# Kernel tuning notes

Measured on AMD Instinct MI355X. Metric: run time of the kernel, lower is better.

The kernel has to match this reference:

```python
import jax, jax.numpy as jnp
import numpy as np

B, M, K, KNN = 2, 256, 64, 16
CXYZ, CFEAT = 3, 61
CIN = CXYZ + CFEAT  # 64
MLPS = [64, 128]
SUMM = sum(MLPS)    # 192
CALIB = 64
EXP = [256, 512]
OUT = 256
EPS = 1e-5


def bn(x, g, b):
    # BatchNorm eval mode with running_mean=0, running_var=1 (channel axis 1)
    shape = (1, -1) + (1,) * (x.ndim - 2)
    return x * (g / jnp.sqrt(1.0 + EPS)).reshape(shape) + b.reshape(shape)


def knn(x, k):
    xx = jnp.sum(x * x, axis=1)                      # (B, N)
    inner = jnp.einsum('bcn,bcm->bnm', x, x)         # (B, N, N)
    pd = 2.0 * inner - xx[:, :, None] - xx[:, None, :]
    return jax.lax.top_k(pd, k)[1]                   # (B, N, k)


def graph_feature(x, idx):
    # x: (B, C, N), idx: (B, N, k) -> (B, 2C, N, k)
    xt = jnp.transpose(x, (0, 2, 1))                 # (B, N, C)
    nb = jax.vmap(lambda a, i: a[i])(xt, idx)        # (B, N, k, C)
    ctr = xt[:, :, None, :]
    feat = jnp.concatenate([nb - ctr, jnp.broadcast_to(ctr, nb.shape)], axis=-1)
    return jnp.transpose(feat, (0, 3, 1, 2))


def forward(xyz, feats, e1_w, e1_g, e1_b, e2_w, e2_g, e2_b,
            cal1_w, cal1_g, cal1_b, cal2_w, cal2_bias,
            exp1_w, exp1_g, exp1_b, exp2_w, exp2_g, exp2_b,
            red_w, red_g, red_b, sc1_w, sc1_b, sc2_w, sc2_b,
            sc_n1_g, sc_n1_b, sc_n2_g, sc_n2_b):
    x3 = xyz.reshape(B * M, K, CXYZ).transpose(0, 2, 1)      # (BM, 3, K)
    f = feats.reshape(B * M, K, CFEAT).transpose(0, 2, 1)    # (BM, 61, K)
    idx = knn(x3, KNN)                                        # USE_FEATS_DIS=False: knn once on xyz
    x = jnp.concatenate([x3, f], axis=1)                      # (BM, 64, K)
    outs = []
    for W, g, b in ((e1_w, e1_g, e1_b), (e2_w, e2_g, e2_b)):
        gf = graph_feature(x, idx)                            # (BM, 2C, K, knn)
        y = jax.nn.relu(bn(jnp.einsum('oc,bcnk->bonk', W, gf), g, b))
        x = y.max(axis=-1)                                    # (BM, mlp_i, K)
        outs.append(x)
    x = jnp.concatenate(outs, axis=1)                         # (BM, 192, K)
    c = jax.nn.relu(bn(jnp.einsum('oc,bcn->bon', cal1_w, x), cal1_g, cal1_b))
    c = jnp.einsum('oc,bcn->bon', cal2_w, c) + cal2_bias[None, :, None]
    x = jax.nn.sigmoid(c) * x
    x = jax.nn.relu(bn(jnp.einsum('oc,bcn->bon', exp1_w, x), exp1_g, exp1_b))
    x = jax.nn.relu(bn(jnp.einsum('oc,bcn->bon', exp2_w, x), exp2_g, exp2_b))
    x = x.max(axis=-1).reshape(B, M, EXP[1]).transpose(0, 2, 1)  # (B, 512, M)
    x = jax.nn.relu(bn(jnp.einsum('oc,bcm->bom', red_w, x), red_g, red_b))
    x = bn(x + x, sc_n1_g, sc_n1_b)
    h = jax.nn.relu(jnp.einsum('oc,bcm->bom', sc1_w, x) + sc1_b[None, :, None])
    h = jnp.einsum('oc,bcm->bom', sc2_w, h) + sc2_b[None, :, None]
    x = bn(x + h, sc_n2_g, sc_n2_b)
    return x                                                  # (B, 256, M)


def setup_inputs() -> dict:
    key = jax.random.key(0)
    ks = jax.random.split(key, 16)
    w = lambda k, s: jax.random.normal(k, s, jnp.float32) * 0.05
    ones = lambda n: jnp.ones((n,), jnp.float32)
    zeros = lambda n: jnp.zeros((n,), jnp.float32)
    return {
        'xyz': jax.random.normal(ks[0], (B, M, K, CXYZ), jnp.float32),
        'feats': jax.random.normal(ks[1], (B, M, K, CFEAT), jnp.float32),
        'e1_w': w(ks[2], (MLPS[0], 2 * CIN)), 'e1_g': ones(MLPS[0]), 'e1_b': zeros(MLPS[0]),
        'e2_w': w(ks[3], (MLPS[1], 2 * MLPS[0])), 'e2_g': ones(MLPS[1]), 'e2_b': zeros(MLPS[1]),
        'cal1_w': w(ks[4], (CALIB, SUMM)), 'cal1_g': ones(CALIB), 'cal1_b': zeros(CALIB),
        'cal2_w': w(ks[5], (SUMM, CALIB)), 'cal2_bias': zeros(SUMM),
        'exp1_w': w(ks[6], (EXP[0], SUMM)), 'exp1_g': ones(EXP[0]), 'exp1_b': zeros(EXP[0]),
        'exp2_w': w(ks[7], (EXP[1], EXP[0])), 'exp2_g': ones(EXP[1]), 'exp2_b': zeros(EXP[1]),
        'red_w': w(ks[8], (OUT, EXP[1])), 'red_g': ones(OUT), 'red_b': zeros(OUT),
        'sc1_w': w(ks[9], (OUT, OUT)), 'sc1_b': zeros(OUT),
        'sc2_w': w(ks[10], (OUT, OUT)), 'sc2_b': zeros(OUT),
        'sc_n1_g': ones(OUT), 'sc_n1_b': zeros(OUT),
        'sc_n2_g': ones(OUT), 'sc_n2_b': zeros(OUT),
    }


def reference(xyz, feats, e1_w, e1_g, e1_b, e2_w, e2_g, e2_b,
              cal1_w, cal1_g, cal1_b, cal2_w, cal2_bias,
              exp1_w, exp1_g, exp1_b, exp2_w, exp2_g, exp2_b,
              red_w, red_g, red_b, sc1_w, sc1_b, sc2_w, sc2_b,
              sc_n1_g, sc_n1_b, sc_n2_g, sc_n2_b):
    return forward(xyz, feats, e1_w, e1_g, e1_b, e2_w, e2_g, e2_b,
                   cal1_w, cal1_g, cal1_b, cal2_w, cal2_bias,
                   exp1_w, exp1_g, exp1_b, exp2_w, exp2_g, exp2_b,
                   red_w, red_g, red_b, sc1_w, sc1_b, sc2_w, sc2_b,
                   sc_n1_g, sc_n1_b, sc_n2_g, sc_n2_b)
```

## Files before the change

kernel.cpp:

```cpp
#include <hip/hip_runtime.h>
#include <hip/hip_bf16.h>
#include <math.h>
#include <stddef.h>

#define DEV __device__ __forceinline__
__device__ const float BNS = 0.99999500003749968f;

typedef __bf16 bf16x8 __attribute__((ext_vector_type(8)));
typedef float  f32x4  __attribute__((ext_vector_type(4)));

DEV unsigned short f2bs(float v){
  union{ __hip_bfloat16 b; unsigned short u; } c; c.b=__float2bfloat16(v); return c.u;
}
DEV float bs2f(unsigned short u){
  union{ unsigned short u; __hip_bfloat16 b; } c; c.u=u; return __bfloat162float(c.b);
}


__global__ __launch_bounds__(256) void k_prep(const float* __restrict__ e1_w,
    const float* __restrict__ e2_w, const float* __restrict__ cal1_w,
    const float* __restrict__ cal2_w, const float* __restrict__ exp1_w,
    const float* __restrict__ exp2_w, unsigned short* __restrict__ Whi,
    unsigned short* __restrict__ Wlo,
    const float* __restrict__ red_w, const float* __restrict__ sc1_w,
    const float* __restrict__ sc2_w, float* __restrict__ Wt_red,
    float* __restrict__ Wt_s1, float* __restrict__ Wt_s2){
  __shared__ float s[32][33];
  int bid = blockIdx.x;
  if(bid < 896){
    const float* src; unsigned short *hi,*lo; int mode, O=0, i0;
    if(bid<32)      { src=e1_w;  hi=Whi;       lo=Wlo;       mode=1; O= 64; i0=bid*256; }
    else if(bid<96) { src=e2_w;  hi=Whi+8192;  lo=Wlo+8192;  mode=1; O=128; i0=(bid-32)*256; }
    else if(bid<144){ src=cal1_w;hi=Whi+24576; lo=Wlo+24576; mode=0;        i0=(bid-96)*256; }
    else if(bid<192){ src=cal2_w;hi=Whi+36864; lo=Wlo+36864; mode=0;        i0=(bid-144)*256; }
    else if(bid<384){ src=exp1_w;hi=Whi+49152; lo=Wlo+49152; mode=0;        i0=(bid-192)*256; }
    else            { src=exp2_w;hi=Whi+98304; lo=Wlo+98304; mode=0;        i0=(bid-384)*256; }
    int i = i0 + threadIdx.x;
    float v;
    if(mode==0) v = src[i];
    else {
      int row=i>>6, c=i&63;
      v = (row<O) ? src[row*128+c] : (src[(row-O)*128+64+c]-src[(row-O)*128+c]);
    }
    unsigned short h=f2bs(v); hi[i]=h; lo[i]=f2bs(v-bs2f(h));
  } else {
    int lb = bid-896;
    const float* in; float* out; int O,K;
    if(lb<128){ in=red_w; out=Wt_red; O=256; K=512; }
    else if(lb<192){ in=sc1_w; out=Wt_s1; O=256; K=256; lb-=128; }
    else { in=sc2_w; out=Wt_s2; O=256; K=256; lb-=192; }
    int nt=O>>5;
    int to=lb%nt, tk=lb/nt;
    int c=threadIdx.x&31, r8=threadIdx.x>>5;
    #pragma unroll
    for(int p=0;p<4;p++){
      int r=r8+p*8;
      s[r][c]=in[(size_t)(to*32+r)*K + tk*32 + c];
    }
    __syncthreads();
    #pragma unroll
    for(int p=0;p<4;p++){
      int r=r8+p*8;
      out[(size_t)(tk*32+r)*O + to*32 + c]=s[c][r];
    }
  }
}

__global__ __launch_bounds__(256) void k_knne12(const float* __restrict__ xyz,
    const float* __restrict__ feats,
    const unsigned short* __restrict__ W1h, const unsigned short* __restrict__ W1l,
    const unsigned short* __restrict__ W2h, const unsigned short* __restrict__ W2l,
    int* __restrict__ idxo, const float* __restrict__ g1, const float* __restrict__ b1,
    const float* __restrict__ g2, const float* __restrict__ b2,
    unsigned short* __restrict__ cat){
  __shared__ float bufA[64*65];
  __shared__ float bufB[64*65];
  __shared__ __align__(16) unsigned short sb[64*136];
  __shared__ int   ips[64*16];
  __shared__ float sx0[64], sx1[64], sx2[64], sxx[64];
  int bm = blockIdx.x;
  int tid = threadIdx.x, n = tid&63, s = tid>>6;
  int wid = tid>>6, lane = tid&63;
  int l15 = lane&15, q = lane>>4;
  if(s==0){
    const float* xp = xyz + (size_t)(bm*64+n)*3;
    float px=xp[0], py=xp[1], pz=xp[2];
    sx0[n]=px; sx1[n]=py; sx2[n]=pz; sxx[n]=px*px+py*py+pz*pz;
  }
  __syncthreads();
  {
    int p = lane>>2, seg = lane&3;
    int n1 = wid*16 + p;
    float px=sx0[n1], py=sx1[n1], pz=sx2[n1], xxn=sxx[n1];
    float pdr[16];
    #pragma unroll
    for(int t=0;t<16;t++){
      int m = seg*16+t;
      pdr[t] = 2.f*(px*sx0[m]+py*sx1[m]+pz*sx2[m]) - xxn - sxx[m];
    }
    for(int j=0;j<16;j++){
      float bv=-3.4e38f; int bi=seg*16;
      #pragma unroll
      for(int t=0;t<16;t++){ if(pdr[t]>bv){bv=pdr[t]; bi=seg*16+t;} }
      float ov=__shfl_xor(bv,1); int oi=__shfl_xor(bi,1);
      if(ov>bv || (ov==bv && oi<bi)){bv=ov;bi=oi;}
      ov=__shfl_xor(bv,2); oi=__shfl_xor(bi,2);
      if(ov>bv || (ov==bv && oi<bi)){bv=ov;bi=oi;}
      if(seg==0) ips[n1*16+j]=bi;
      if((bi>>4)==seg) pdr[bi&15]=-3.4e38f;
    }
  }
  {
    unsigned short* r = sb + n*136;
    if(s==0){
      float px=sx0[n], py=sx1[n], pz=sx2[n];
      unsigned short h;
      h=f2bs(px); r[0]=h; r[64]=f2bs(px-bs2f(h));
      h=f2bs(py); r[1]=h; r[65]=f2bs(py-bs2f(h));
      h=f2bs(pz); r[2]=h; r[66]=f2bs(pz-bs2f(h));
    }
    const float* fp = feats + (size_t)(bm*64+n)*61;
    #pragma unroll
    for(int t=0;t<16;t++){
      int cc = s*16+t;
      if(cc<61){
        float v=fp[cc]; unsigned short h=f2bs(v);
        r[3+cc]=h; r[64+3+cc]=f2bs(v-bs2f(h));
      }
    }
  }
  __syncthreads();
  #pragma unroll
  for(int t=0;t<4;t++) idxo[bm*1024 + tid*4 + t] = ips[tid*4 + t];
  {
    int rbase = ((wid<2)?0:64) + (wid&1)*32;
    f32x4 acc[2][4];
    #pragma unroll
    for(int a=0;a<2;a++)
      #pragma unroll
      for(int d=0;d<4;d++) acc[a][d]=(f32x4){0.f,0.f,0.f,0.f};
    #pragma unroll
    for(int kc=0;kc<2;kc++){
      int k0=kc*32;
      size_t a0=(size_t)(rbase+l15)*64 + k0 + q*8;
      size_t a1=(size_t)(rbase+16+l15)*64 + k0 + q*8;
      bf16x8 a0h=*(const bf16x8*)(W1h+a0), a0l=*(const bf16x8*)(W1l+a0);
      bf16x8 a1h=*(const bf16x8*)(W1h+a1), a1l=*(const bf16x8*)(W1l+a1);
      #pragma unroll
      for(int nt=0;nt<4;nt++){
        int row = nt*16 + l15;
        bf16x8 bh = *(const bf16x8*)&sb[row*136 + k0 + q*8];
        bf16x8 bl = *(const bf16x8*)&sb[row*136 + 64 + k0 + q*8];
        acc[0][nt]=__builtin_amdgcn_mfma_f32_16x16x32_bf16(a0h,bh,acc[0][nt],0,0,0);
        acc[0][nt]=__builtin_amdgcn_mfma_f32_16x16x32_bf16(a0h,bl,acc[0][nt],0,0,0);
        acc[0][nt]=__builtin_amdgcn_mfma_f32_16x16x32_bf16(a0l,bh,acc[0][nt],0,0,0);
        acc[1][nt]=__builtin_amdgcn_mfma_f32_16x16x32_bf16(a1h,bh,acc[1][nt],0,0,0);
        acc[1][nt]=__builtin_amdgcn_mfma_f32_16x16x32_bf16(a1h,bl,acc[1][nt],0,0,0);
        acc[1][nt]=__builtin_amdgcn_mfma_f32_16x16x32_bf16(a1l,bh,acc[1][nt],0,0,0);
      }
    }
    __syncthreads();
    float* dst = (wid<2)? bufA : bufB;
    int ro = (wid&1)*32;
    #pragma unroll
    for(int mt=0;mt<2;mt++)
      #pragma unroll
      for(int nt=0;nt<4;nt++)
        #pragma unroll
        for(int rr=0;rr<4;rr++)
          dst[(ro+mt*16+q*4+rr)*65 + nt*16+l15] = acc[mt][nt][rr];
  }
  __syncthreads();
  {
    int o = lane;
    float sc = g1[o]*BNS, bi = b1[o];
    #pragma unroll 4
    for(int j=0;j<16;j++){
      int nn = wid*16 + j;
      const int* ip = &ips[nn*16];
      float mz = -3.4e38f;
      #pragma unroll
      for(int k=0;k<16;k++) mz = fmaxf(mz, bufA[o*65 + ip[k]]);
      float v = fmaxf(sc*(mz + bufB[o*65 + nn]) + bi, 0.f);
      unsigned short hv = f2bs(v), lv = f2bs(v - bs2f(hv));
      size_t cb = ((size_t)bm*64+nn)*384 + o;
      cat[cb] = hv; cat[cb+192] = lv;
      sb[nn*136 + o] = hv; sb[nn*136 + 64 + o] = lv;
    }
  }
  for(int ch=0; ch<2; ch++){
    __syncthreads();
    int rbase = ((wid<2)?0:128) + ch*64 + (wid&1)*32;
    f32x4 acc[2][4];
    #pragma unroll
    for(int a=0;a<2;a++)
      #pragma unroll
      for(int d=0;d<4;d++) acc[a][d]=(f32x4){0.f,0.f,0.f,0.f};
    #pragma unroll
    for(int kc=0;kc<2;kc++){
      int k0=kc*32;
      size_t a0=(size_t)(rbase+l15)*64 + k0 + q*8;
      size_t a1=(size_t)(rbase+16+l15)*64 + k0 + q*8;
      bf16x8 a0h=*(const bf16x8*)(W2h+a0), a0l=*(const bf16x8*)(W2l+a0);
      bf16x8 a1h=*(const bf16x8*)(W2h+a1), a1l=*(const bf16x8*)(W2l+a1);
      #pragma unroll
      for(int nt=0;nt<4;nt++){
        int row = nt*16 + l15;
        bf16x8 bh = *(const bf16x8*)&sb[row*136 + k0 + q*8];
        bf16x8 bl = *(const bf16x8*)&sb[row*136 + 64 + k0 + q*8];
        acc[0][nt]=__builtin_amdgcn_mfma_f32_16x16x32_bf16(a0h,bh,acc[0][nt],0,0,0);
        acc[0][nt]=__builtin_amdgcn_mfma_f32_16x16x32_bf16(a0h,bl,acc[0][nt],0,0,0);
        acc[0][nt]=__builtin_amdgcn_mfma_f32_16x16x32_bf16(a0l,bh,acc[0][nt],0,0,0);
        acc[1][nt]=__builtin_amdgcn_mfma_f32_16x16x32_bf16(a1h,bh,acc[1][nt],0,0,0);
        acc[1][nt]=__builtin_amdgcn_mfma_f32_16x16x32_bf16(a1h,bl,acc[1][nt],0,0,0);
        acc[1][nt]=__builtin_amdgcn_mfma_f32_16x16x32_bf16(a1l,bh,acc[1][nt],0,0,0);
      }
    }
    __syncthreads();
    float* dst = (wid<2)? bufA : bufB;
    int ro = (wid&1)*32;
    #pragma unroll
    for(int mt=0;mt<2;mt++)
      #pragma unroll
      for(int nt=0;nt<4;nt++)
        #pragma unroll
        for(int rr=0;rr<4;rr++)
          dst[(ro+mt*16+q*4+rr)*65 + nt*16+l15] = acc[mt][nt][rr];
    __syncthreads();
    int o = ch*64 + lane;
    float sc = g2[o]*BNS, bi = b2[o];
    #pragma unroll 4
    for(int j=0;j<16;j++){
      int nn = wid*16 + j;
      const int* ip = &ips[nn*16];
      float mz = -3.4e38f;
      #pragma unroll
      for(int k=0;k<16;k++) mz = fmaxf(mz, bufA[lane*65 + ip[k]]);
      float v = fmaxf(sc*(mz + bufB[lane*65 + nn]) + bi, 0.f);
      unsigned short hv = f2bs(v);
      size_t cb = ((size_t)bm*64+nn)*384 + 64 + o;
      cat[cb] = hv; cat[cb+192] = f2bs(v - bs2f(hv));
    }
  }
}

__global__ __launch_bounds__(256) void k_cal(
    const unsigned short* __restrict__ Whi, const unsigned short* __restrict__ Wlo,
    unsigned short* __restrict__ cats,
    const float* __restrict__ c1g, const float* __restrict__ c1b,
    const float* __restrict__ c2bias){
  const unsigned short* c1w_h = Whi+24576; const unsigned short* c1w_l = Wlo+24576;
  const unsigned short* c2w_h = Whi+36864; const unsigned short* c2w_l = Wlo+36864;
  __shared__ __align__(16) unsigned short sW[64*64];
  __shared__ __align__(16) unsigned short sX[128*64];
  __shared__ __align__(16) unsigned short c1L[128*136];
  int rt = blockIdx.x;
  int tid = threadIdx.x, wid = tid>>6, lane = tid&63;
  int l15 = lane&15, q = lane>>4;
  f32x4 acc1[8];
  #pragma unroll
  for(int d=0;d<8;d++) acc1[d]=(f32x4){0.f,0.f,0.f,0.f};
  size_t xbase = (size_t)rt*128*384;
  for(int kc=0;kc<6;kc++){
    int k0=kc*32;
    __syncthreads();
    #pragma unroll
    for(int i=0;i<2;i++){
      int U = tid + i*256;
      int r = U>>3, up = U&7, u = up ^ (r&7);
      const unsigned short* src = (u<4)
        ? (c1w_h + (size_t)r*192 + k0 + u*8)
        : (c1w_l + (size_t)r*192 + k0 + (u-4)*8);
      *(uint4*)&sW[U*8] = *(const uint4*)src;
    }
    #pragma unroll
    for(int i=0;i<4;i++){
      int U = tid + i*256;
      int r = U>>3, up = U&7, u = up ^ (r&7);
      const unsigned short* src = cats + xbase + (size_t)r*384
        + (u<4 ? (size_t)(k0 + u*8) : (size_t)(192 + k0 + (u-4)*8));
      *(uint4*)&sX[U*8] = *(const uint4*)src;
    }
    __syncthreads();
    int o = wid*16 + l15;
    bf16x8 wh = *(const bf16x8*)&sW[(o*8 + ((  q) ^ (o&7)))*8];
    bf16x8 wl = *(const bf16x8*)&sW[(o*8 + ((4+q) ^ (o&7)))*8];
    #pragma unroll
    for(int nf=0;nf<8;nf++){
      int r = nf*16 + l15;
      bf16x8 xh = *(const bf16x8*)&sX[(r*8 + ((  q) ^ (r&7)))*8];
      bf16x8 xl = *(const bf16x8*)&sX[(r*8 + ((4+q) ^ (r&7)))*8];
      acc1[nf]=__builtin_amdgcn_mfma_f32_16x16x32_bf16(wh,xh,acc1[nf],0,0,0);
      acc1[nf]=__builtin_amdgcn_mfma_f32_16x16x32_bf16(wh,xl,acc1[nf],0,0,0);
      acc1[nf]=__builtin_amdgcn_mfma_f32_16x16x32_bf16(wl,xh,acc1[nf],0,0,0);
    }
  }
  {
    int ob0 = wid*16 + q*4;
    float s0[4], b0[4];
    #pragma unroll
    for(int r=0;r<4;r++){ s0[r]=c1g[ob0+r]*BNS; b0[r]=c1b[ob0+r]; }
    #pragma unroll
    for(int nf=0;nf<8;nf++){
      int n = nf*16 + l15;
      unsigned short hv[4], lv[4];
      #pragma unroll
      for(int r=0;r<4;r++){
        float v = fmaxf(acc1[nf][r]*s0[r]+b0[r], 0.f);
        hv[r]=f2bs(v); lv[r]=f2bs(v - bs2f(hv[r]));
      }
      *(ushort4*)&c1L[n*136 + ob0]      = make_ushort4(hv[0],hv[1],hv[2],hv[3]);
      *(ushort4*)&c1L[n*136 + 64 + ob0] = make_ushort4(lv[0],lv[1],lv[2],lv[3]);
    }
  }
  __syncthreads();
  f32x4 acc2[3][8];
  #pragma unroll
  for(int a=0;a<3;a++)
    #pragma unroll
    for(int d=0;d<8;d++) acc2[a][d]=(f32x4){0.f,0.f,0.f,0.f};
  #pragma unroll
  for(int kc=0;kc<2;kc++){
    int k0=kc*32;
    bf16x8 ah[3], al[3];
    #pragma unroll
    for(int mt=0;mt<3;mt++){
      int o = wid*48 + mt*16 + l15;
      ah[mt]=*(const bf16x8*)(c2w_h + (size_t)o*64 + k0 + q*8);
      al[mt]=*(const bf16x8*)(c2w_l + (size_t)o*64 + k0 + q*8);
    }
    #pragma unroll
    for(int nf=0;nf<8;nf++){
      int n = nf*16 + l15;
      bf16x8 bh = *(const bf16x8*)&c1L[n*136 + k0 + q*8];
      bf16x8 bl = *(const bf16x8*)&c1L[n*136 + 64 + k0 + q*8];
      #pragma unroll
      for(int mt=0;mt<3;mt++){
        acc2[mt][nf]=__builtin_amdgcn_mfma_f32_16x16x32_bf16(ah[mt],bh,acc2[mt][nf],0,0,0);
        acc2[mt][nf]=__builtin_amdgcn_mfma_f32_16x16x32_bf16(ah[mt],bl,acc2[mt][nf],0,0,0);
        acc2[mt][nf]=__builtin_amdgcn_mfma_f32_16x16x32_bf16(al[mt],bh,acc2[mt][nf],0,0,0);
      }
    }
  }
  #pragma unroll
  for(int mt=0;mt<3;mt++){
    int ob0 = wid*48 + mt*16 + q*4;
    float bi[4];
    #pragma unroll
    for(int r=0;r<4;r++) bi[r]=c2bias[ob0+r];
    #pragma unroll
    for(int nf=0;nf<8;nf++){
      size_t row = (size_t)rt*128 + nf*16 + l15;
      size_t rb = row*384;
      ushort4 hv = *(ushort4*)(cats + rb + ob0);
      ushort4 lv = *(ushort4*)(cats + rb + 192 + ob0);
      unsigned short h[4]={hv.x,hv.y,hv.z,hv.w}, l[4]={lv.x,lv.y,lv.z,lv.w};
      #pragma unroll
      for(int r=0;r<4;r++){
        float g = 1.f/(1.f+__expf(-(acc2[mt][nf][r]+bi[r])));
        float f = (bs2f(h[r])+bs2f(l[r]))*g;
        h[r]=f2bs(f); l[r]=f2bs(f-bs2f(h[r]));
      }
      *(ushort4*)(cats + rb + ob0)       = make_ushort4(h[0],h[1],h[2],h[3]);
      *(ushort4*)(cats + rb + 192 + ob0) = make_ushort4(l[0],l[1],l[2],l[3]);
    }
  }
}

template<int K, int BO, int EPI>
__global__ __launch_bounds__(256) void k_mm2(
    const unsigned short* __restrict__ Whi, const unsigned short* __restrict__ Wlo,
    const unsigned short* __restrict__ X, void* __restrict__ Og,
    const float* __restrict__ sg, const float* __restrict__ bg, int O){
  constexpr int WO = BO/4;
  constexpr int MT = WO/16;
  constexpr int WUNITS = BO*8;
  __shared__ __align__(16) unsigned short sW[BO*64];
  __shared__ __align__(16) unsigned short sX[128*64];
  int rt = blockIdx.x;
  int o0 = blockIdx.y*BO;
  int tid = threadIdx.x, wid = tid>>6, lane = tid&63;
  int l15 = lane&15, q = lane>>4;
  f32x4 acc[MT][8];
  #pragma unroll
  for(int a=0;a<MT;a++)
    #pragma unroll
    for(int d=0;d<8;d++) acc[a][d]=(f32x4){0.f,0.f,0.f,0.f};
  size_t xbase = (size_t)rt*128*2*K;
  for(int kc=0; kc<K/32; kc++){
    int k0 = kc*32;
    __syncthreads();
    #pragma unroll
    for(int i=0;i<WUNITS/256;i++){
      int U = tid + i*256;
      int r = U>>3, up = U&7, u = up ^ (r&7);
      const unsigned short* src = (u<4)
        ? (Whi + (size_t)(o0+r)*K + k0 + u*8)
        : (Wlo + (size_t)(o0+r)*K + k0 + (u-4)*8);
      *(uint4*)&sW[U*8] = *(const uint4*)src;
    }
    #pragma unroll
    for(int i=0;i<4;i++){
      int U = tid + i*256;
      int r = U>>3, up = U&7, u = up ^ (r&7);
      const unsigned short* src = X + xbase + (size_t)r*2*K
        + (u<4 ? (size_t)(k0 + u*8) : (size_t)(K + k0 + (u-4)*8));
      *(uint4*)&sX[U*8] = *(const uint4*)src;
    }
    __syncthreads();
    bf16x8 wf[MT][2];
    #pragma unroll
    for(int mt=0;mt<MT;mt++){
      int o = wid*WO + mt*16 + l15;
      wf[mt][0] = *(const bf16x8*)&sW[(o*8 + ((  q) ^ (o&7)))*8];
      wf[mt][1] = *(const bf16x8*)&sW[(o*8 + ((4+q) ^ (o&7)))*8];
    }
    #pragma unroll
    for(int nf=0;nf<8;nf++){
      int r = nf*16 + l15;
      bf16x8 xh = *(const bf16x8*)&sX[(r*8 + ((  q) ^ (r&7)))*8];
      bf16x8 xl = *(const bf16x8*)&sX[(r*8 + ((4+q) ^ (r&7)))*8];
      #pragma unroll
      for(int mt=0;mt<MT;mt++){
        acc[mt][nf]=__builtin_amdgcn_mfma_f32_16x16x32_bf16(wf[mt][0],xh,acc[mt][nf],0,0,0);
        acc[mt][nf]=__builtin_amdgcn_mfma_f32_16x16x32_bf16(wf[mt][0],xl,acc[mt][nf],0,0,0);
        acc[mt][nf]=__builtin_amdgcn_mfma_f32_16x16x32_bf16(wf[mt][1],xh,acc[mt][nf],0,0,0);
      }
    }
  }
  if(EPI==0){
    unsigned short* ob = (unsigned short*)Og;
    #pragma unroll
    for(int mt=0;mt<MT;mt++){
      int ob0 = o0 + wid*WO + mt*16 + q*4;
      float s0[4], b0[4];
      #pragma unroll
      for(int r=0;r<4;r++){ s0[r]=sg[ob0+r]*BNS; b0[r]=bg[ob0+r]; }
      #pragma unroll
      for(int nf=0;nf<8;nf++){
        size_t row = (size_t)rt*128 + nf*16 + l15;
        size_t rb = row*2*O;
        unsigned short hv[4], lv[4];
        #pragma unroll
        for(int r=0;r<4;r++){
          float v = fmaxf(acc[mt][nf][r]*s0[r]+b0[r], 0.f);
          hv[r]=f2bs(v); lv[r]=f2bs(v - bs2f(hv[r]));
        }
        *(ushort4*)(ob + rb + ob0)     = make_ushort4(hv[0],hv[1],hv[2],hv[3]);
        *(ushort4*)(ob + rb + O + ob0) = make_ushort4(lv[0],lv[1],lv[2],lv[3]);
      }
    }
  } else {
    float* pool = (float*)Og;
    #pragma unroll
    for(int mt=0;mt<MT;mt++){
      int ob0 = o0 + wid*WO + mt*16 + q*4;
      #pragma unroll
      for(int half=0;half<2;half++){
        int bm = 2*rt + half;
        int b = bm>>8, m = bm&255;
        #pragma unroll
        for(int r=0;r<4;r++){
          float s=sg[ob0+r]*BNS, bi=bg[ob0+r];
          float v = acc[mt][half*4+0][r]*s+bi;
          v = fmaxf(v, acc[mt][half*4+1][r]*s+bi);
          v = fmaxf(v, acc[mt][half*4+2][r]*s+bi);
          v = fmaxf(v, acc[mt][half*4+3][r]*s+bi);
          v = fmaxf(v, 0.f);
          v = fmaxf(v, __shfl_xor(v,1));
          v = fmaxf(v, __shfl_xor(v,2));
          v = fmaxf(v, __shfl_xor(v,4));
          v = fmaxf(v, __shfl_xor(v,8));
          if(l15==0) pool[((size_t)b*512 + ob0+r)*256 + m] = v;
        }
      }
    }
  }
}

template<int EPI>
__global__ __launch_bounds__(256) void k_head(const float* __restrict__ Wt,
    const float* __restrict__ Xg, float* __restrict__ Og,
    const float* __restrict__ p0, const float* __restrict__ p1,
    const float* __restrict__ p2, const float* __restrict__ p3,
    const float* __restrict__ res, int O, int K){
  __shared__ float As[32][64];
  __shared__ float Bs[32][32];
  int not_ = O>>6;
  int g = blockIdx.x / not_, ot = blockIdx.x % not_;
  int b = g>>3, mg = g&7;
  int o0 = ot*64;
  int tid=threadIdx.x, tx=tid&7, ty=tid>>3;
  float acc[2][4];
  #pragma unroll
  for(int a=0;a<2;a++)
    #pragma unroll
    for(int d=0;d<4;d++) acc[a][d]=0.f;
  const float* Xb = Xg + (size_t)b*K*256 + mg*32;
  for(int k0=0;k0<K;k0+=32){
    __syncthreads();
    #pragma unroll
    for(int p=0;p<2;p++){
      int r = p*16 + (tid>>4), c4 = (tid&15)*4;
      *(float4*)&As[r][c4] = *(const float4*)&Wt[(size_t)(k0+r)*O + o0 + c4];
    }
    {
      int r = tid>>3, c4 = (tid&7)*4;
      *(float4*)&Bs[r][c4] = *(const float4*)&Xb[(size_t)(k0+r)*256 + c4];
    }
    __syncthreads();
    #pragma unroll
    for(int k=0;k<32;k++){
      float av[2], bv[4];
      av[0]=As[k][ty*2]; av[1]=As[k][ty*2+1];
      #pragma unroll
      for(int d=0;d<4;d++) bv[d]=Bs[k][tx*4+d];
      #pragma unroll
      for(int a=0;a<2;a++)
        #pragma unroll
        for(int d=0;d<4;d++) acc[a][d]+=av[a]*bv[d];
    }
  }
  int m0 = mg*32 + tx*4;
  #pragma unroll
  for(int a=0;a<2;a++){
    int o=o0+ty*2+a;
    float* orow = Og + ((size_t)b*O + o)*256 + m0;
    float v[4];
    if(EPI==0){
      float s=p0[o]*BNS, bi=p1[o], s1=p2[o]*BNS, b1=p3[o];
      #pragma unroll
      for(int d=0;d<4;d++){ float r=fmaxf(acc[a][d]*s+bi,0.f); v[d]=2.f*r*s1+b1; }
    } else if(EPI==1){
      float bi=p0[o];
      #pragma unroll
      for(int d=0;d<4;d++) v[d]=fmaxf(acc[a][d]+bi,0.f);
    } else {
      float bi=p0[o], s2=p1[o]*BNS, b2=p2[o];
      const float* rr = res + ((size_t)b*O + o)*256 + m0;
      #pragma unroll
      for(int d=0;d<4;d++){ float u=rr[d]+acc[a][d]+bi; v[d]=u*s2+b2; }
    }
    *(float4*)orow = make_float4(v[0],v[1],v[2],v[3]);
  }
}

extern "C" void kernel_launch(void* const* d_in, const int* in_sizes, int n_in,
                              void* d_out, int out_size, void* d_ws, size_t ws_size,
                              hipStream_t stream){
  const float* xyz     =(const float*)d_in[0];
  const float* feats   =(const float*)d_in[1];
  const float* e1_w    =(const float*)d_in[2];
  const float* e1_g    =(const float*)d_in[3];
  const float* e1_b    =(const float*)d_in[4];
  const float* e2_w    =(const float*)d_in[5];
  const float* e2_g    =(const float*)d_in[6];
  const float* e2_b    =(const float*)d_in[7];
  const float* cal1_w  =(const float*)d_in[8];
  const float* cal1_g  =(const float*)d_in[9];
  const float* cal1_b  =(const float*)d_in[10];
  const float* cal2_w  =(const float*)d_in[11];
  const float* cal2_bias=(const float*)d_in[12];
  const float* exp1_w  =(const float*)d_in[13];
  const float* exp1_g  =(const float*)d_in[14];
  const float* exp1_b  =(const float*)d_in[15];
  const float* exp2_w  =(const float*)d_in[16];
  const float* exp2_g  =(const float*)d_in[17];
  const float* exp2_b  =(const float*)d_in[18];
  const float* red_w   =(const float*)d_in[19];
  const float* red_g   =(const float*)d_in[20];
  const float* red_b   =(const float*)d_in[21];
  const float* sc1_w   =(const float*)d_in[22];
  const float* sc1_b   =(const float*)d_in[23];
  const float* sc2_w   =(const float*)d_in[24];
  const float* sc2_b   =(const float*)d_in[25];
  const float* sc_n1_g =(const float*)d_in[26];
  const float* sc_n1_b =(const float*)d_in[27];
  const float* sc_n2_g =(const float*)d_in[28];
  const float* sc_n2_b =(const float*)d_in[29];

  char* wsb=(char*)d_ws;
  int*            idx =(int*)           (wsb);
  unsigned short* cats=(unsigned short*)(wsb + 10485760);
  unsigned short* p1s =(unsigned short*)(wsb + 35651584);
  float*          pool=(float*)         (wsb + 69206016);
  float*          x1  =(float*)         (wsb + 70254592);
  float*          hbuf=(float*)         (wsb + 70778880);
  unsigned short* Whi =(unsigned short*)(wsb + 75497472);
  unsigned short* Wlo =(unsigned short*)(wsb + 76021760);
  float*          Wt_red=(float*)       (wsb + 76546048);
  float*          Wt_s1 =(float*)       (wsb + 77070336);
  float*          Wt_s2 =(float*)       (wsb + 77332480);
  unsigned short* e1e_h=Whi;          unsigned short* e1e_l=Wlo;
  unsigned short* e2e_h=Whi+8192;     unsigned short* e2e_l=Wlo+8192;
  unsigned short* e1w_h=Whi+49152;    unsigned short* e1w_l=Wlo+49152;
  unsigned short* e2w_h=Whi+98304;    unsigned short* e2w_l=Wlo+98304;

  k_prep      <<<1152,256,0,stream>>>(e1_w,e2_w,cal1_w,cal2_w,exp1_w,exp2_w,Whi,Wlo,
                                      red_w,sc1_w,sc2_w,Wt_red,Wt_s1,Wt_s2);
  k_knne12    <<<512,256,0,stream>>>(xyz,feats,e1e_h,e1e_l,e2e_h,e2e_l,idx,
                                     e1_g,e1_b,e2_g,e2_b,cats);
  k_cal       <<<256,256,0,stream>>>(Whi,Wlo,cats,cal1_g,cal1_b,cal2_bias);
  k_mm2<192,128,0><<<dim3(256,2),256,0,stream>>>(e1w_h,e1w_l,cats,(void*)p1s,exp1_g,exp1_b,256);
  k_mm2<256,128,2><<<dim3(256,4),256,0,stream>>>(e2w_h,e2w_l,p1s,(void*)pool,exp2_g,exp2_b,512);
  k_head<0>   <<< 64,256,0,stream>>>(Wt_red,pool,x1,  red_g,red_b,sc_n1_g,sc_n1_b,nullptr,256,512);
  k_head<1>   <<< 64,256,0,stream>>>(Wt_s1, x1,  hbuf,sc1_b,nullptr,nullptr,nullptr,nullptr,256,256);
  k_head<2>   <<< 64,256,0,stream>>>(Wt_s2, hbuf,(float*)d_out,sc2_b,sc_n2_g,sc_n2_b,nullptr,x1,256,256);
}
```

Before: 267.8 us.

## Fuse three head GEMM kernels into one per-column-group kernel

Replaces the three k_head launches (reduce, sc1, sc2) with a single kernel. Each block handles 4 point columns for one batch, keeps the intermediate activations in shared memory, and each thread computes one output channel across the three layers. This removes two launches and the global round trips for x1/hbuf. In exchange each block re-reads the full weight matrices (128 blocks each streaming about 1M floats of weights), so there is much less weight reuse than the tiled GEMMs had.

```diff
diff --git a/kernel.cpp b/kernel.cpp
--- a/kernel.cpp
+++ b/kernel.cpp
@@ -478,70 +478,69 @@
   }
 }
 
-template<int EPI>
-__global__ __launch_bounds__(256) void k_head(const float* __restrict__ Wt,
-    const float* __restrict__ Xg, float* __restrict__ Og,
-    const float* __restrict__ p0, const float* __restrict__ p1,
-    const float* __restrict__ p2, const float* __restrict__ p3,
-    const float* __restrict__ res, int O, int K){
-  __shared__ float As[32][64];
-  __shared__ float Bs[32][32];
-  int not_ = O>>6;
-  int g = blockIdx.x / not_, ot = blockIdx.x % not_;
-  int b = g>>3, mg = g&7;
-  int o0 = ot*64;
-  int tid=threadIdx.x, tx=tid&7, ty=tid>>3;
-  float acc[2][4];
+__global__ __launch_bounds__(256) void k_headf(const float* __restrict__ Wt_red,
+    const float* __restrict__ Wt_s1, const float* __restrict__ Wt_s2,
+    const float* __restrict__ pool, float* __restrict__ Og,
+    const float* __restrict__ red_g, const float* __restrict__ red_b,
+    const float* __restrict__ n1g, const float* __restrict__ n1b,
+    const float* __restrict__ s1b, const float* __restrict__ s2b,
+    const float* __restrict__ n2g, const float* __restrict__ n2b){
+  __shared__ float P[512*5];
+  __shared__ float X1[256*5];
+  __shared__ float H[256*5];
+  int g = blockIdx.x;
+  int b = g>>6, mg = g&63;
+  int m0 = mg*4;
+  int o = threadIdx.x;
   #pragma unroll
-  for(int a=0;a<2;a++)
-    #pragma unroll
-    for(int d=0;d<4;d++) acc[a][d]=0.f;
-  const float* Xb = Xg + (size_t)b*K*256 + mg*32;
-  for(int k0=0;k0<K;k0+=32){
-    __syncthreads();
-    #pragma unroll
-    for(int p=0;p<2;p++){
-      int r = p*16 + (tid>>4), c4 = (tid&15)*4;
-      *(float4*)&As[r][c4] = *(const float4*)&Wt[(size_t)(k0+r)*O + o0 + c4];
-    }
-    {
-      int r = tid>>3, c4 = (tid&7)*4;
-      *(float4*)&Bs[r][c4] = *(const float4*)&Xb[(size_t)(k0+r)*256 + c4];
-    }
-    __syncthreads();
-    #pragma unroll
-    for(int k=0;k<32;k++){
-      float av[2], bv[4];
-      av[0]=As[k][ty*2]; av[1]=As[k][ty*2+1];
-      #pragma unroll
-      for(int d=0;d<4;d++) bv[d]=Bs[k][tx*4+d];
-      #pragma unroll
-      for(int a=0;a<2;a++)
-        #pragma unroll
-        for(int d=0;d<4;d++) acc[a][d]+=av[a]*bv[d];
-    }
-  }
-  int m0 = mg*32 + tx*4;
-  #pragma unroll
-  for(int a=0;a<2;a++){
-    int o=o0+ty*2+a;
-    float* orow = Og + ((size_t)b*O + o)*256 + m0;
+  for(int i=0;i<2;i++){
+    int c = o + i*256;
+    float4 v = *(const float4*)&pool[((size_t)b*512+c)*256 + m0];
+    P[c*5+0]=v.x; P[c*5+1]=v.y; P[c*5+2]=v.z; P[c*5+3]=v.w;
+  }
+  __syncthreads();
+  float acc[4];
+  acc[0]=acc[1]=acc[2]=acc[3]=0.f;
+  for(int c=0;c<512;c++){
+    float w = Wt_red[c*256+o];
+    #pragma unroll
+    for(int j=0;j<4;j++) acc[j] += w*P[c*5+j];
+  }
+  float x1r[4];
+  {
+    float s=red_g[o]*BNS, bi=red_b[o], s1=n1g[o]*BNS, b1=n1b[o];
+    #pragma unroll
+    for(int j=0;j<4;j++){
+      float r=fmaxf(acc[j]*s+bi,0.f);
+      x1r[j]=2.f*r*s1+b1;
+      X1[o*5+j]=x1r[j];
+    }
+  }
+  __syncthreads();
+  acc[0]=acc[1]=acc[2]=acc[3]=0.f;
+  for(int c=0;c<256;c++){
+    float w = Wt_s1[c*256+o];
+    #pragma unroll
+    for(int j=0;j<4;j++) acc[j] += w*X1[c*5+j];
+  }
+  {
+    float bi=s1b[o];
+    #pragma unroll
+    for(int j=0;j<4;j++) H[o*5+j]=fmaxf(acc[j]+bi,0.f);
+  }
+  __syncthreads();
+  acc[0]=acc[1]=acc[2]=acc[3]=0.f;
+  for(int c=0;c<256;c++){
+    float w = Wt_s2[c*256+o];
+    #pragma unroll
+    for(int j=0;j<4;j++) acc[j] += w*H[c*5+j];
+  }
+  {
+    float bi=s2b[o], s2=n2g[o]*BNS, b2=n2b[o];
     float v[4];
-    if(EPI==0){
-      float s=p0[o]*BNS, bi=p1[o], s1=p2[o]*BNS, b1=p3[o];
-      #pragma unroll
-      for(int d=0;d<4;d++){ float r=fmaxf(acc[a][d]*s+bi,0.f); v[d]=2.f*r*s1+b1; }
-    } else if(EPI==1){
-      float bi=p0[o];
-      #pragma unroll
-      for(int d=0;d<4;d++) v[d]=fmaxf(acc[a][d]+bi,0.f);
-    } else {
-      float bi=p0[o], s2=p1[o]*BNS, b2=p2[o];
-      const float* rr = res + ((size_t)b*O + o)*256 + m0;
-      #pragma unroll
-      for(int d=0;d<4;d++){ float u=rr[d]+acc[a][d]+bi; v[d]=u*s2+b2; }
-    }
-    *(float4*)orow = make_float4(v[0],v[1],v[2],v[3]);
+    #pragma unroll
+    for(int j=0;j<4;j++){ float u=x1r[j]+acc[j]+bi; v[j]=u*s2+b2; }
+    *(float4*)&Og[((size_t)b*256+o)*256 + m0] = make_float4(v[0],v[1],v[2],v[3]);
   }
 }
 
@@ -584,8 +583,6 @@
   unsigned short* cats=(unsigned short*)(wsb + 10485760);
   unsigned short* p1s =(unsigned short*)(wsb + 35651584);
   float*          pool=(float*)         (wsb + 69206016);
-  float*          x1  =(float*)         (wsb + 70254592);
-  float*          hbuf=(float*)         (wsb + 70778880);
   unsigned short* Whi =(unsigned short*)(wsb + 75497472);
   unsigned short* Wlo =(unsigned short*)(wsb + 76021760);
   float*          Wt_red=(float*)       (wsb + 76546048);
@@ -603,7 +600,6 @@
   k_cal       <<<256,256,0,stream>>>(Whi,Wlo,cats,cal1_g,cal1_b,cal2_bias);
   k_mm2<192,128,0><<<dim3(256,2),256,0,stream>>>(e1w_h,e1w_l,cats,(void*)p1s,exp1_g,exp1_b,256);
   k_mm2<256,128,2><<<dim3(256,4),256,0,stream>>>(e2w_h,e2w_l,p1s,(void*)pool,exp2_g,exp2_b,512);
-  k_head<0>   <<< 64,256,0,stream>>>(Wt_red,pool,x1,  red_g,red_b,sc_n1_g,sc_n1_b,nullptr,256,512);
-  k_head<1>   <<< 64,256,0,stream>>>(Wt_s1, x1,  hbuf,sc1_b,nullptr,nullptr,nullptr,nullptr,256,256);
-  k_head<2>   <<< 64,256,0,stream>>>(Wt_s2, hbuf,(float*)d_out,sc2_b,sc_n2_g,sc_n2_b,nullptr,x1,256,256);
-}
+  k_headf     <<<128,256,0,stream>>>(Wt_red,Wt_s1,Wt_s2,pool,(float*)d_out,
+                                     red_g,red_b,sc_n1_g,sc_n1_b,sc1_b,sc2_b,sc_n2_g,sc_n2_b);
+}
```

After: 270.7 us. About the same (+1.1%).
